# Optimization experiments

Measured on AMD Instinct MI355X. Metric: run time of the kernel, lower is better.

Reference implementation:

```python
import jax, jax.numpy as jnp
import numpy as np

NG, NF, NW = 5, 10, 4
STEP = 1 + NG + NF            # 16 signatures per writer
B = NW * STEP                 # 64
T, DFEAT = 512, 64
GAMMA = 5.0                   # SoftDTW gamma
BANDWIDTH = 0.1               # Sakoe-Chiba band (|i-j| <= 0.1 -> diagonal only)
INF = 1e7                     # finite 'infinity' to keep grads NaN-free
ALPHA, BETA, P_W, R_W = 0.5, 1.0, 0.1, 0.1
MARGIN_MAX, MARGIN_MIN = 1.0, 0.1
K_NUM, K_MUL = 5, 2.0
SIZ = NW * (NW + 1) // 2      # 10 (buffer size in original code)


def setup_inputs() -> dict:
    key = jax.random.key(0)
    k1, k2 = jax.random.split(key)
    data = jax.random.normal(k1, (B, T, DFEAT), dtype=jnp.float32)
    teacher_data = jax.random.normal(k2, (B, T, DFEAT), dtype=jnp.float32)
    # equal lengths: the bandwidth=0.1 band only admits the main diagonal,
    # so only equal-length pairs yield finite SoftDTW values.
    lens = jnp.full((B,), T, dtype=jnp.int32)
    return {"data": data, "lens": lens, "teacher_data": teacher_data}


def sq_dist(X, Y):
    # X: [P,N,d], Y: [P,M,d] -> [P,N,M] squared euclidean cost (SoftDTW default)
    x2 = jnp.sum(X * X, -1)[:, :, None]
    y2 = jnp.sum(Y * Y, -1)[:, None, :]
    return x2 + y2 - 2.0 * jnp.einsum('bid,bjd->bij', X, Y)


def softdtw_batch(Dmat):
    # Batched SoftDTW via anti-diagonal wavefront scan. Dmat: [P,N,N].
    Pn, N, _ = Dmat.shape
    i = jnp.arange(N)
    k = jnp.arange(2 * N - 1)[:, None]            # diagonal index
    j = k - i[None, :]                            # [2N-1, N]
    valid = (j >= 0) & (j < N)
    inband = valid & (jnp.abs(i[None, :] - j) <= BANDWIDTH)
    jc = jnp.clip(j, 0, N - 1)
    Dg = Dmat[:, i[None, :], jc]                  # [P, 2N-1, N] diag-gathered costs
    Dg = jnp.moveaxis(Dg, 1, 0)                   # [2N-1, P, N]

    def step(carry, xs):
        Rp, Rp2 = carry                           # diagonals k-1, k-2; [P,N]
        Dk, mk, kk = xs
        pad = jnp.full((Pn, 1), INF, Dk.dtype)
        above = jnp.concatenate([pad, Rp[:, :-1]], axis=1)   # R[i-1, j]
        left = Rp                                             # R[i, j-1]
        diag = jnp.concatenate([pad, Rp2[:, :-1]], axis=1)   # R[i-1, j-1]
        stacked = jnp.stack([above, left, diag], axis=0)
        smin = -GAMMA * jax.nn.logsumexp(-stacked / GAMMA, axis=0)
        Rk = Dk + smin
        Rk = jnp.where(kk == 0, Dk, Rk)           # R[0,0] = D[0,0]
        Rk = jnp.where(mk[None, :], Rk, INF)      # outside band -> INF
        return (Rk, Rp), None

    init = (jnp.full((Pn, N), INF, Dmat.dtype), jnp.full((Pn, N), INF, Dmat.dtype))
    (Rlast, _), _ = jax.lax.scan(step, init, (Dg, inband, jnp.arange(2 * N - 1)))
    return Rlast[:, N - 1]                        # R[N-1, N-1]


def mmd_loss(src, tgt):
    # Literal multi-kernel Gaussian MMD applied to 3D [n,T,d] inputs:
    # torch broadcasting of ((total[None]-total[:,None])**2).sum(2) -> [2n,2n,d]
    n = src.shape[0]
    total = jnp.concatenate([src, tgt], axis=0)   # [2n, T, d]
    sq = jnp.sum(total * total, axis=1)           # [2n, d]
    cross = jnp.einsum('atd,btd->abd', total, total)
    L2 = sq[:, None, :] + sq[None, :, :] - 2.0 * cross
    ns = 2 * n
    bw = jax.lax.stop_gradient(jnp.sum(L2)) / (ns * ns - ns)  # .data in torch
    bw = bw / (K_MUL ** (K_NUM // 2))
    kernels = sum(jnp.exp(-L2 / (bw * (K_MUL ** ii))) for ii in range(K_NUM))
    XX, YY = kernels[:n, :n], kernels[n:, n:]
    XY, YX = kernels[:n, n:], kernels[n:, :n]
    return jnp.mean(XX + YY - XY - YX)


def reference(data, lens, teacher_data):
    lens_f = lens.astype(data.dtype)
    widx = jnp.arange(NW) * STEP
    a_idx = jnp.repeat(widx, NG + NF)                                   # anchors
    o_idx = (widx[:, None] + 1 + jnp.arange(NG + NF)[None, :]).reshape(-1)
    # batch student + teacher pairs into one SoftDTW call: [2P, T, T]
    X = jnp.concatenate([data[a_idx], teacher_data[a_idx]], axis=0)
    Y = jnp.concatenate([data[o_idx], teacher_data[o_idx]], axis=0)
    sd = softdtw_batch(sq_dist(X, Y))
    denom = lens_f[a_idx] + lens_f[o_idx]
    Pn = NW * (NG + NF)
    d_s = (sd[:Pn] / denom).reshape(NW, NG + NF)
    d_t = (sd[Pn:] / denom).reshape(NW, NG + NF)
    dist_g, dist_n = d_s[:, :NG], d_s[:, NG:]
    dist_g_t, dist_n_t = d_t[:, :NG], d_t[:, NG:]

    # teacher-driven dynamic margin
    dists_t = jax.nn.relu(dist_n_t[:, :, None] - dist_g_t[:, None, :])  # [NW,NF,NG]
    mx = jnp.max(dists_t, axis=(1, 2), keepdims=True)
    fd = (MARGIN_MAX - MARGIN_MIN) / mx * dists_t + MARGIN_MIN
    lk = jax.nn.relu(dist_g[:, None, :] - dist_n[:, :, None] + fd)
    nz = jax.lax.stop_gradient(jnp.sum(lk != 0, axis=(1, 2))).astype(lk.dtype)
    lv = jnp.sum(lk, axis=(1, 2)) / (nz + 1.0)
    ca = jnp.mean(dist_g, axis=1)
    cb = jnp.mean(dist_n[:, :5], axis=1)
    intra = jnp.sum(dist_g - ca[:, None], axis=1)
    inter = jax.nn.relu(BETA - jnp.abs(ca - cb))
    total_loss = jnp.mean(lv + intra * P_W + inter * R_W)

    # MMD over writer pairs, excluding last 5 (random forgeries)
    groups = data.reshape(NW, STEP, T, DFEAT)[:, :STEP - 5]             # [NW,11,T,d]
    pairs = [(i, j) for i in range(NW) for j in range(1, NW) if i != j]
    src = jnp.stack([groups[i] for i, _ in pairs])
    tgt = jnp.stack([groups[j] for _, j in pairs])
    mmd_vals = jax.vmap(mmd_loss)(src, tgt)
    mmds = jnp.zeros((SIZ,), data.dtype).at[:len(pairs)].set(mmd_vals)
    mmd1 = jnp.max(mmds) * ALPHA
    return total_loss + mmd1
```

## Files before the change

kernel.cpp:

```cpp
#include <hip/hip_runtime.h>
#include <math.h>

#define T_LEN 512
#define DF 64
#define ROW_ELEMS (T_LEN * DF)
#define STEP_ 16
#define NROWS_G 44
#define GSTRIDE (NROWS_G * DF)

__constant__ int c_PI[9] = {0, 0, 0, 1, 1, 2, 2, 3, 3};
__constant__ int c_PJ[9] = {1, 2, 3, 2, 3, 1, 3, 1, 2};

__device__ inline float blockSum(float v, float* tmp4) {
    #pragma unroll
    for (int off = 32; off > 0; off >>= 1) v += __shfl_down(v, off);
    if ((threadIdx.x & 63) == 0) tmp4[threadIdx.x >> 6] = v;
    __syncthreads();
    const float s = tmp4[0] + tmp4[1] + tmp4[2] + tmp4[3];
    __syncthreads();
    return s;
}

__global__ __launch_bounds__(256) void k_pair(const float* __restrict__ data,
                                              const float* __restrict__ teacher,
                                              float* __restrict__ sd,
                                              float* __restrict__ G0,
                                              float* __restrict__ G1,
                                              unsigned* __restrict__ counter)
{
    const int b = blockIdx.x;
    const int tid = threadIdx.x;

    __shared__ float red2[16][16][DF];
    __shared__ float redS[256];

    if (b == 0 && tid == 0) *counter = 0u;

    if (b < 132) {
        const int tile = b >> 1, half = b & 1;
        int q = tile, ta = 0;
        while (q >= 11 - ta) { q -= 11 - ta; ta++; }
        const int tb = ta + q;
        const int ty = tid >> 4, dq = tid & 15;
        const int ua0 = ta * 4, ub0 = tb * 4;

        const float4* rA[4];
        const float4* rB[4];
        #pragma unroll
        for (int i = 0; i < 4; ++i) {
            const int ua = ua0 + i, ub = ub0 + i;
            rA[i] = (const float4*)(data + (size_t)((ua / 11) * STEP_ + (ua % 11)) * ROW_ELEMS);
            rB[i] = (const float4*)(data + (size_t)((ub / 11) * STEP_ + (ub % 11)) * ROW_ELEMS);
        }

        float acc[4][4][4];
        #pragma unroll
        for (int i = 0; i < 4; ++i)
            #pragma unroll
            for (int j = 0; j < 4; ++j)
                #pragma unroll
                for (int c = 0; c < 4; ++c) acc[i][j][c] = 0.f;

        const int tbase = half * 256 + ty;
        #pragma unroll 2
        for (int it = 0; it < 16; ++it) {
            const int t = tbase + it * 16;
            float4 av[4], bv[4];
            #pragma unroll
            for (int i = 0; i < 4; ++i) av[i] = rA[i][t * 16 + dq];
            #pragma unroll
            for (int j = 0; j < 4; ++j) bv[j] = rB[j][t * 16 + dq];
            #pragma unroll
            for (int i = 0; i < 4; ++i)
                #pragma unroll
                for (int j = 0; j < 4; ++j) {
                    acc[i][j][0] += av[i].x * bv[j].x;
                    acc[i][j][1] += av[i].y * bv[j].y;
                    acc[i][j][2] += av[i].z * bv[j].z;
                    acc[i][j][3] += av[i].w * bv[j].w;
                }
        }

        #pragma unroll
        for (int i = 0; i < 4; ++i)
            #pragma unroll
            for (int j = 0; j < 4; ++j)
                *(float4*)&red2[ty][i * 4 + j][dq * 4] =
                    make_float4(acc[i][j][0], acc[i][j][1], acc[i][j][2], acc[i][j][3]);
        __syncthreads();

        float* __restrict__ Gh = half ? G1 : G0;
        for (int o = tid; o < 1024; o += 256) {
            const int ij = o >> 6, d = o & 63;
            float s = 0.f;
            #pragma unroll
            for (int t2 = 0; t2 < 16; ++t2) s += red2[t2][ij][d];
            const int ua = ua0 + (ij >> 2), ub = ub0 + (ij & 3);
            Gh[(size_t)ua * GSTRIDE + ub * DF + d] = s;
            Gh[(size_t)ub * GSTRIDE + ua * DF + d] = s;
        }
    } else {
        const int bb = b - 132;
        const float* src = (bb < 60) ? data : teacher;
        const int p = bb % 60;
        const int w = p / 15, k = p % 15;
        const float4* A = (const float4*)(src + (size_t)(w * STEP_) * ROW_ELEMS);
        const float4* O = (const float4*)(src + (size_t)(w * STEP_ + 1 + k) * ROW_ELEMS);
        float acc = 0.f;
        #pragma unroll 4
        for (int i = tid; i < ROW_ELEMS / 4; i += 256) {
            float4 a = A[i], o = O[i];
            float dx = a.x - o.x, dy = a.y - o.y, dz = a.z - o.z, dw = a.w - o.w;
            acc += dx * dx + dy * dy + dz * dz + dw * dw;
        }
        redS[tid] = acc;
        __syncthreads();
        for (int s = 128; s > 0; s >>= 1) {
            if (tid < s) redS[tid] += redS[tid + s];
            __syncthreads();
        }
        if (tid == 0) sd[bb] = redS[0];
    }
}

__global__ __launch_bounds__(256) void k_mmd2(const float* __restrict__ G0,
                                              const float* __restrict__ G1,
                                              const float* __restrict__ sd,
                                              const int* __restrict__ lens,
                                              float* __restrict__ partial,
                                              unsigned* __restrict__ counter,
                                              float* __restrict__ out)
{
    const int blk = blockIdx.x;
    const int p = blk / 22, aa = blk % 22;
    const int tid = threadIdx.x;
    const int gi = c_PI[p], gj = c_PJ[p];

    __shared__ float diagT[22 * DF];
    __shared__ float tmp4[4];
    __shared__ float fin[256];
    __shared__ float mmd9[9];
    __shared__ float sdl[120];
    __shared__ int lastFlag;

    for (int e = tid; e < 22 * DF; e += 256) {
        const int bb = e >> 6, d2 = e & 63;
        const int ub = (bb < 11) ? gi * 11 + bb : gj * 11 + bb - 11;
        const size_t off = (size_t)ub * GSTRIDE + ub * DF + d2;
        diagT[e] = G0[off] + G1[off];
    }

    const float4* G0q = (const float4*)G0;
    const float4* G1q = (const float4*)G1;
    float gs = 0.f;
    for (int e = tid; e < 7744; e += 256) {
        const int f4 = e % 176;
        const int sp = (e / 176) & 1;
        const int a2 = e / 352;
        const int ua = (a2 < 11) ? gi * 11 + a2 : gj * 11 + a2 - 11;
        const int colbase = (sp ? gj : gi) * 11 * DF;
        const size_t qi = ((size_t)ua * GSTRIDE + colbase) / 4 + f4;
        const float4 v0 = G0q[qi], v1 = G1q[qi];
        gs += (v0.x + v1.x) + (v0.y + v1.y) + (v0.z + v1.z) + (v0.w + v1.w);
    }
    __syncthreads();

    float dsp = 0.f;
    for (int e = tid; e < 22 * DF; e += 256) dsp += diagT[e];

    const float sumG    = blockSum(gs,  tmp4);
    const float diagSum = blockSum(dsp, tmp4);

    const float bw = (44.f * diagSum - 2.f * sumG) / (462.f * 4.f);
    const float inv0 = 1.f / bw;

    const int ua = (aa < 11) ? gi * 11 + aa : gj * 11 + aa - 11;
    const bool sa = (aa < 11);
    const float4* cr0 = (const float4*)(G0 + (size_t)ua * GSTRIDE);
    const float4* cr1 = (const float4*)(G1 + (size_t)ua * GSTRIDE);
    const float4* dTq = (const float4*)diagT;

    float s2 = 0.f;
    for (int e = tid; e < 22 * 16; e += 256) {
        const int bb = e >> 4, dq = e & 15;
        const int ub = (bb < 11) ? gi * 11 + bb : gj * 11 + bb - 11;
        const float4 c0 = cr0[ub * 16 + dq], c1 = cr1[ub * 16 + dq];
        const float4 dB = dTq[e];
        const float4 dA = dTq[aa * 16 + dq];
        float l2[4];
        l2[0] = dA.x + dB.x - 2.f * (c0.x + c1.x);
        l2[1] = dA.y + dB.y - 2.f * (c0.y + c1.y);
        l2[2] = dA.z + dB.z - 2.f * (c0.z + c1.z);
        l2[3] = dA.w + dB.w - 2.f * (c0.w + c1.w);
        float kv = 0.f;
        #pragma unroll
        for (int c = 0; c < 4; ++c) {
            float inv = inv0;
            #pragma unroll
            for (int ii = 0; ii < 5; ++ii) { kv += __expf(-l2[c] * inv); inv *= 0.5f; }
        }
        s2 += ((bb < 11) == sa) ? kv : -kv;
    }
    const float rowSum = blockSum(s2, tmp4);

    if (tid == 0) {
        partial[blk] = rowSum;
        __threadfence();
        const unsigned old = atomicAdd(counter, 1u);
        lastFlag = (old == 197u);
    }
    __syncthreads();
    if (!lastFlag) return;

    float pv = 0.f;
    if (tid < 198) pv = atomicAdd(&partial[tid], 0.f);
    fin[tid] = pv;
    __syncthreads();

    if (tid < 9) {
        float s = 0.f;
        #pragma unroll
        for (int k2 = 0; k2 < 22; ++k2) s += fin[tid * 22 + k2];
        mmd9[tid] = s / (121.f * 64.f);
    }
    if (tid < 120) sdl[tid] = sd[tid];
    __syncthreads();

    if (tid == 0) {
        float total = 0.f;
        for (int w = 0; w < 4; ++w) {
            float ds[15], dt[15];
            for (int k = 0; k < 15; ++k) {
                const float denom = (float)lens[w * STEP_] + (float)lens[w * STEP_ + 1 + k];
                ds[k] = sdl[w * 15 + k] / denom;
                dt[k] = sdl[60 + w * 15 + k] / denom;
            }
            float mx = 0.f;
            for (int i = 0; i < 10; ++i)
                for (int j = 0; j < 5; ++j) {
                    float v = dt[5 + i] - dt[j];
                    v = v > 0.f ? v : 0.f;
                    mx = fmaxf(mx, v);
                }
            const float scale = (1.0f - 0.1f) / mx;
            float sum_lk = 0.f, nz = 0.f;
            for (int i = 0; i < 10; ++i)
                for (int j = 0; j < 5; ++j) {
                    float v = dt[5 + i] - dt[j];
                    v = v > 0.f ? v : 0.f;
                    const float fd = scale * v + 0.1f;
                    float lk = ds[j] - ds[5 + i] + fd;
                    lk = lk > 0.f ? lk : 0.f;
                    sum_lk += lk;
                    if (lk != 0.f) nz += 1.f;
                }
            const float lv = sum_lk / (nz + 1.f);
            const float ca = (ds[0] + ds[1] + ds[2] + ds[3] + ds[4]) * 0.2f;
            const float cb = (ds[5] + ds[6] + ds[7] + ds[8] + ds[9]) * 0.2f;
            const float intra = (ds[0] - ca) + (ds[1] - ca) + (ds[2] - ca) + (ds[3] - ca) + (ds[4] - ca);
            float inter = 1.0f - fabsf(ca - cb);
            inter = inter > 0.f ? inter : 0.f;
            total += lv + intra * 0.1f + inter * 0.1f;
        }
        total *= 0.25f;

        float mmax = 0.f;
        for (int q2 = 0; q2 < 9; ++q2) mmax = fmaxf(mmax, mmd9[q2]);
        out[0] = total + 0.5f * mmax;
    }
}

extern "C" void kernel_launch(void* const* d_in, const int* in_sizes, int n_in,
                              void* d_out, int out_size, void* d_ws, size_t ws_size,
                              hipStream_t stream) {
    const float* data    = (const float*)d_in[0];
    const int*   lens    = (const int*)d_in[1];
    const float* teacher = (const float*)d_in[2];
    float* out = (float*)d_out;

    float*    sd      = (float*)d_ws;
    float*    G0      = sd + 128;
    float*    G1      = G0 + (size_t)NROWS_G * GSTRIDE;
    float*    partial = G1 + (size_t)NROWS_G * GSTRIDE;
    unsigned* counter = (unsigned*)(partial + 256);

    k_pair<<<252, 256, 0, stream>>>(data, teacher, sd, G0, G1, counter);
    k_mmd2<<<9 * 22, 256, 0, stream>>>(G0, G1, sd, lens, partial, counter, out);
}
```

Baseline: 102.1 us.

## Merge per-row MMD blocks into one 1024-thread block per writer pair

The MMD kernel now runs 9 blocks of 1024 threads, one per writer pair, where it used to run 198 blocks of 256 threads, one per (pair, row). Each block computes the whole 22x22 kernel sum itself. This removes the bandwidth statistics and diagonal setup that 22 blocks per pair each recomputed, and shrinks the final cross-block reduction to 9 partials. The cost is far fewer blocks on a GPU with many CUs, so there is less parallelism and latency hiding for the exp-heavy main loop.

```diff
diff --git a/kernel.cpp b/kernel.cpp
--- a/kernel.cpp
+++ b/kernel.cpp
@@ -11,12 +11,18 @@
 __constant__ int c_PI[9] = {0, 0, 0, 1, 1, 2, 2, 3, 3};
 __constant__ int c_PJ[9] = {1, 2, 3, 2, 3, 1, 3, 1, 2};
 
-__device__ inline float blockSum(float v, float* tmp4) {
+__device__ inline float loadF(float* p) {
+    return __hip_atomic_load(p, __ATOMIC_RELAXED, __HIP_MEMORY_SCOPE_AGENT);
+}
+
+__device__ inline float blockSum16(float v, float* tmp16) {
     #pragma unroll
     for (int off = 32; off > 0; off >>= 1) v += __shfl_down(v, off);
-    if ((threadIdx.x & 63) == 0) tmp4[threadIdx.x >> 6] = v;
-    __syncthreads();
-    const float s = tmp4[0] + tmp4[1] + tmp4[2] + tmp4[3];
+    if ((threadIdx.x & 63) == 0) tmp16[threadIdx.x >> 6] = v;
+    __syncthreads();
+    float s = 0.f;
+    #pragma unroll
+    for (int w = 0; w < 16; ++w) s += tmp16[w];
     __syncthreads();
     return s;
 }
@@ -123,27 +129,25 @@
     }
 }
 
-__global__ __launch_bounds__(256) void k_mmd2(const float* __restrict__ G0,
-                                              const float* __restrict__ G1,
-                                              const float* __restrict__ sd,
-                                              const int* __restrict__ lens,
-                                              float* __restrict__ partial,
-                                              unsigned* __restrict__ counter,
-                                              float* __restrict__ out)
+__global__ __launch_bounds__(1024) void k_mmd3(const float* __restrict__ G0,
+                                               const float* __restrict__ G1,
+                                               float* __restrict__ sd,
+                                               const int* __restrict__ lens,
+                                               float* __restrict__ mmd9,
+                                               unsigned* __restrict__ counter,
+                                               float* __restrict__ out)
 {
     const int blk = blockIdx.x;
-    const int p = blk / 22, aa = blk % 22;
     const int tid = threadIdx.x;
-    const int gi = c_PI[p], gj = c_PJ[p];
+    const int gi = c_PI[blk], gj = c_PJ[blk];
 
     __shared__ float diagT[22 * DF];
-    __shared__ float tmp4[4];
-    __shared__ float fin[256];
-    __shared__ float mmd9[9];
+    __shared__ float tmp16[16];
+    __shared__ float mmd9l[9];
     __shared__ float sdl[120];
     __shared__ int lastFlag;
 
-    for (int e = tid; e < 22 * DF; e += 256) {
+    for (int e = tid; e < 22 * DF; e += 1024) {
         const int bb = e >> 6, d2 = e & 63;
         const int ub = (bb < 11) ? gi * 11 + bb : gj * 11 + bb - 11;
         const size_t off = (size_t)ub * GSTRIDE + ub * DF + d2;
@@ -153,7 +157,7 @@
     const float4* G0q = (const float4*)G0;
     const float4* G1q = (const float4*)G1;
     float gs = 0.f;
-    for (int e = tid; e < 7744; e += 256) {
+    for (int e = tid; e < 7744; e += 1024) {
         const int f4 = e % 176;
         const int sp = (e / 176) & 1;
         const int a2 = e / 352;
@@ -166,26 +170,25 @@
     __syncthreads();
 
     float dsp = 0.f;
-    for (int e = tid; e < 22 * DF; e += 256) dsp += diagT[e];
-
-    const float sumG    = blockSum(gs,  tmp4);
-    const float diagSum = blockSum(dsp, tmp4);
+    for (int e = tid; e < 22 * DF; e += 1024) dsp += diagT[e];
+
+    const float sumG    = blockSum16(gs,  tmp16);
+    const float diagSum = blockSum16(dsp, tmp16);
 
     const float bw = (44.f * diagSum - 2.f * sumG) / (462.f * 4.f);
     const float inv0 = 1.f / bw;
 
-    const int ua = (aa < 11) ? gi * 11 + aa : gj * 11 + aa - 11;
-    const bool sa = (aa < 11);
-    const float4* cr0 = (const float4*)(G0 + (size_t)ua * GSTRIDE);
-    const float4* cr1 = (const float4*)(G1 + (size_t)ua * GSTRIDE);
     const float4* dTq = (const float4*)diagT;
-
     float s2 = 0.f;
-    for (int e = tid; e < 22 * 16; e += 256) {
-        const int bb = e >> 4, dq = e & 15;
+    for (int e = tid; e < 7744; e += 1024) {
+        const int aa = e / 352;
+        const int rest = e % 352;
+        const int bb = rest >> 4, dq = rest & 15;
+        const int ua = (aa < 11) ? gi * 11 + aa : gj * 11 + aa - 11;
         const int ub = (bb < 11) ? gi * 11 + bb : gj * 11 + bb - 11;
-        const float4 c0 = cr0[ub * 16 + dq], c1 = cr1[ub * 16 + dq];
-        const float4 dB = dTq[e];
+        const size_t ci = ((size_t)ua * GSTRIDE) / 4 + ub * 16 + dq;
+        const float4 c0 = G0q[ci], c1 = G1q[ci];
+        const float4 dB = dTq[bb * 16 + dq];
         const float4 dA = dTq[aa * 16 + dq];
         float l2[4];
         l2[0] = dA.x + dB.x - 2.f * (c0.x + c1.x);
@@ -199,31 +202,21 @@
             #pragma unroll
             for (int ii = 0; ii < 5; ++ii) { kv += __expf(-l2[c] * inv); inv *= 0.5f; }
         }
-        s2 += ((bb < 11) == sa) ? kv : -kv;
-    }
-    const float rowSum = blockSum(s2, tmp4);
+        s2 += (((aa < 11) == (bb < 11)) ? kv : -kv);
+    }
+    const float pairSum = blockSum16(s2, tmp16);
 
     if (tid == 0) {
-        partial[blk] = rowSum;
+        mmd9[blk] = pairSum / (121.f * 64.f);
         __threadfence();
         const unsigned old = atomicAdd(counter, 1u);
-        lastFlag = (old == 197u);
+        lastFlag = (old == 8u);
     }
     __syncthreads();
     if (!lastFlag) return;
 
-    float pv = 0.f;
-    if (tid < 198) pv = atomicAdd(&partial[tid], 0.f);
-    fin[tid] = pv;
-    __syncthreads();
-
-    if (tid < 9) {
-        float s = 0.f;
-        #pragma unroll
-        for (int k2 = 0; k2 < 22; ++k2) s += fin[tid * 22 + k2];
-        mmd9[tid] = s / (121.f * 64.f);
-    }
-    if (tid < 120) sdl[tid] = sd[tid];
+    if (tid < 9)   mmd9l[tid] = loadF(&mmd9[tid]);
+    if (tid < 120) sdl[tid]  = sd[tid];
     __syncthreads();
 
     if (tid == 0) {
@@ -265,7 +258,7 @@
         total *= 0.25f;
 
         float mmax = 0.f;
-        for (int q2 = 0; q2 < 9; ++q2) mmax = fmaxf(mmax, mmd9[q2]);
+        for (int q2 = 0; q2 < 9; ++q2) mmax = fmaxf(mmax, mmd9l[q2]);
         out[0] = total + 0.5f * mmax;
     }
 }
@@ -281,9 +274,9 @@
     float*    sd      = (float*)d_ws;
     float*    G0      = sd + 128;
     float*    G1      = G0 + (size_t)NROWS_G * GSTRIDE;
-    float*    partial = G1 + (size_t)NROWS_G * GSTRIDE;
-    unsigned* counter = (unsigned*)(partial + 256);
+    float*    mmd9    = G1 + (size_t)NROWS_G * GSTRIDE;
+    unsigned* counter = (unsigned*)(mmd9 + 16);
 
     k_pair<<<252, 256, 0, stream>>>(data, teacher, sd, G0, G1, counter);
-    k_mmd2<<<9 * 22, 256, 0, stream>>>(G0, G1, sd, lens, partial, counter, out);
-}
+    k_mmd3<<<9, 1024, 0, stream>>>(G0, G1, sd, lens, mmd9, counter, out);
+}
```

Result: faster. 99.31 us (-2.7%).
